# Kernel optimization log

Measured on AMD Instinct MI355X. Metric: run time of the kernel, lower is better.

## Reference

```python
import jax, jax.numpy as jnp
import numpy as np

B, T, TM = 4, 1024, 1500
D_MODEL, D_FFN, H, D_HEAD, D_MEM = 1024, 4096, 16, 64, 1024
EPS = 1e-5


def layernorm(x, g):
    m = jnp.mean(x, axis=-1, keepdims=True)
    xc = x - m
    v = jnp.mean(xc * xc, axis=-1, keepdims=True)
    return xc * jax.lax.rsqrt(v + EPS) * g


def setup_inputs() -> dict:
    key = jax.random.key(0)
    ks = jax.random.split(key, 12)
    s = lambda fan_in: 1.0 / np.sqrt(fan_in)
    return {
        "x": jax.random.normal(ks[0], (B, T, D_MODEL), jnp.float32),
        "encoder_output": jax.random.normal(ks[1], (B, TM, D_MEM), jnp.float32),
        "encoder_mask": jax.random.randint(ks[2], (B, TM), 0, 2).astype(bool),
        "w_qkv": jax.random.normal(ks[3], (D_MODEL, 3 * H * D_HEAD), jnp.float32) * s(D_MODEL),
        "w_o_sa": jax.random.normal(ks[4], (H * D_HEAD, D_MODEL), jnp.float32) * s(H * D_HEAD),
        "w_q": jax.random.normal(ks[5], (D_MODEL, H * D_HEAD), jnp.float32) * s(D_MODEL),
        "w_kv": jax.random.normal(ks[6], (D_MEM, 2 * H * D_HEAD), jnp.float32) * s(D_MEM),
        "w_o_xa": jax.random.normal(ks[7], (H * D_HEAD, D_MODEL), jnp.float32) * s(H * D_HEAD),
        "w_ff1": jax.random.normal(ks[8], (D_MODEL, D_FFN), jnp.float32) * s(D_MODEL),
        "w_ff2": jax.random.normal(ks[9], (D_FFN, D_MODEL), jnp.float32) * s(D_FFN),
        "g_sa": jnp.ones((D_MODEL,), jnp.float32),
        "g_xaq": jnp.ones((D_MODEL,), jnp.float32),
        "g_xam": jnp.ones((D_MEM,), jnp.float32),
        "g_ff": jnp.ones((D_MODEL,), jnp.float32),
    }


def reference(x, encoder_output, encoder_mask, w_qkv, w_o_sa, w_q, w_kv, w_o_xa,
              w_ff1, w_ff2, g_sa, g_xaq, g_xam, g_ff):
    b, t, _ = x.shape
    scale = D_HEAD ** -0.5

    # ---- causal self-attention ----
    residual = x
    xn = layernorm(x, g_sa)
    qkv = (xn @ w_qkv).reshape(b, t, 3, H, D_HEAD)
    q, k, v = qkv[:, :, 0], qkv[:, :, 1], qkv[:, :, 2]  # (B,T,H,D)
    scores = jnp.einsum('bqhd,bkhd->bhqk', q, k) * scale
    causal = jnp.tril(jnp.ones((t, t), x.dtype))
    scores = scores + (1.0 - causal) * -1e9
    attn = jax.nn.softmax(scores, axis=-1)
    sa = jnp.einsum('bhqk,bkhd->bqhd', attn, v).reshape(b, t, H * D_HEAD)
    x = residual + sa @ w_o_sa

    # ---- cross-attention ----
    residual = x
    qn = layernorm(x, g_xaq)
    mn = layernorm(encoder_output, g_xam)
    tq, tm = t, mn.shape[1]
    qx = (qn @ w_q).reshape(b, tq, H, D_HEAD)
    kvx = (mn @ w_kv).reshape(b, tm, 2, H, D_HEAD)
    kx, vx = kvx[:, :, 0], kvx[:, :, 1]
    xs = jnp.einsum('bqhd,bkhd->bhqk', qx, kx) * scale
    xs = jnp.where(encoder_mask[:, None, None, :], xs, -jnp.inf)
    xattn = jax.nn.softmax(xs, axis=-1)
    xa = jnp.einsum('bhqk,bkhd->bqhd', xattn, vx).reshape(b, tq, H * D_HEAD)
    x = residual + xa @ w_o_xa

    # ---- pointwise FFN (kernel_size=1 conv == linear) ----
    residual = x
    h = layernorm(x, g_ff)
    h = jax.nn.gelu(h @ w_ff1, approximate=True) @ w_ff2
    x = residual + h
    return (x, k, v)
```

## Files before the change

kernel.cpp:

```cpp
#include <hip/hip_runtime.h>
#include <hip/hip_bf16.h>
#include <cstdint>
#include <cstddef>


typedef __attribute__((ext_vector_type(4))) float f32x4;
typedef __attribute__((ext_vector_type(8))) short s8v;
typedef __attribute__((ext_vector_type(2))) unsigned uint2v;

#define DEVI __device__ __forceinline__

DEVI short f2bf(float f) {
  union { float f; unsigned u; } x; x.f = f;
  unsigned r = x.u + 0x7fffu + ((x.u >> 16) & 1u);
  return (short)(r >> 16);
}
DEVI unsigned cvtpk_bf2(float lo, float hi) {
  unsigned r;
  asm("v_cvt_pk_bf16_f32 %0, %1, %2" : "=v"(r) : "v"(lo), "v"(hi));
  return r;
}
DEVI float fexp2(float x) {
  float r;
  asm("v_exp_f32 %0, %1" : "=v"(r) : "v"(x));
  return r;
}
DEVI float bpermf(int srclane, float v) {
  union { float f; int i; } x; x.f = v;
  x.i = __builtin_amdgcn_ds_bpermute(srclane << 2, x.i);
  return x.f;
}
DEVI void gload_lds16(const void* g, void* l) {
  __builtin_amdgcn_global_load_lds((const __attribute__((address_space(1))) void*)g,
                                   (__attribute__((address_space(3))) void*)l,
                                   16, 0, 0);
}

DEVI void xcd_swizzle(int& bx, int& by) {
  int gx = gridDim.x, gy = gridDim.y;
  int nxy = gx * gy, chunk = nxy >> 3;
  int orig = blockIdx.y * gx + blockIdx.x;
  int gid = (orig & 7) * chunk + (orig >> 3);
  int full = gy << 3, nfull = gx >> 3, lim = nfull * full;
  if (gid < lim) {
    int band = gid / full, r = gid - band * full;
    bx = (band << 3) + (r & 7);
    by = r >> 3;
  } else {
    int r = gid - lim, w = gx - (nfull << 3);
    bx = (nfull << 3) + r % w;
    by = r / w;
  }
}

__global__ __launch_bounds__(256) void k_prep(
    const float* __restrict__ wqkv, const float* __restrict__ wosa,
    const float* __restrict__ wq,   const float* __restrict__ wkv,
    const float* __restrict__ woxa, const float* __restrict__ wff1,
    const float* __restrict__ wff2,
    short* __restrict__ wqkv_t, short* __restrict__ wosa_t,
    short* __restrict__ wq_t,   short* __restrict__ wkv_t,
    short* __restrict__ woxa_t, short* __restrict__ wff1_t,
    short* __restrict__ wff2_t,
    const int* __restrict__ mask, unsigned long long* __restrict__ mbits) {
  int id = blockIdx.x;
  const float* w; short* wt; int K, N, tx, r;
  if (id < 3072)       { w = wqkv; wt = wqkv_t; K = 1024; N = 3072; tx = 96;  r = id; }
  else if (id < 4096)  { w = wosa; wt = wosa_t; K = 1024; N = 1024; tx = 32;  r = id - 3072; }
  else if (id < 5120)  { w = wq;   wt = wq_t;   K = 1024; N = 1024; tx = 32;  r = id - 4096; }
  else if (id < 7168)  { w = wkv;  wt = wkv_t;  K = 1024; N = 2048; tx = 64;  r = id - 5120; }
  else if (id < 8192)  { w = woxa; wt = woxa_t; K = 1024; N = 1024; tx = 32;  r = id - 7168; }
  else if (id < 12288) { w = wff1; wt = wff1_t; K = 1024; N = 4096; tx = 128; r = id - 8192; }
  else if (id < 16384) { w = wff2; wt = wff2_t; K = 4096; N = 1024; tx = 32;  r = id - 12288; }
  else {
    int t = threadIdx.x;
    if (t < 96) {
      int b = t / 24, wd = t % 24;
      unsigned long long v = 0;
      const int* mb = mask + (size_t)b * 1500;
      for (int j = 0; j < 64; j++) {
        int k = wd * 64 + j;
        if (k < 1500 && mb[k]) v |= (1ull << j);
      }
      mbits[b * 24 + wd] = v;
    }
    return;
  }
  __shared__ float tile[32][33];
  int n0 = (r % tx) * 32, k0 = (r / tx) * 32;
  int t = threadIdx.x;
  int row = t >> 3, c4 = (t & 7) * 4;
  *(f32x4*)&tile[row][c4] = *(const f32x4*)(w + (size_t)(k0 + row) * N + n0 + c4);
  __syncthreads();
  float v0 = tile[c4 + 0][row], v1 = tile[c4 + 1][row];
  float v2 = tile[c4 + 2][row], v3 = tile[c4 + 3][row];
  uint2v o = {cvtpk_bf2(v0, v1), cvtpk_bf2(v2, v3)};
  *(uint2v*)(wt + (size_t)(n0 + row) * K + k0 + c4) = o;
}

__global__ __launch_bounds__(256) void k_vtrans(
    const short* __restrict__ src, int srs, int coff,
    short* __restrict__ dst, int T, int Tp) {
  __shared__ short tile[32][72];
  int bh = blockIdx.y, b = bh >> 4, h = bh & 15;
  int t0 = blockIdx.x * 32;
  const short* sB = src + (size_t)b * T * srs + coff + h * 64;
  short* dB = dst + (size_t)bh * 64 * Tp;
  int t = threadIdx.x;
  int r = t >> 3, c = (t & 7) * 8;
  int tr = t0 + r; if (tr > T - 1) tr = T - 1;
  *(s8v*)&tile[r][c] = *(const s8v*)(sB + (size_t)tr * srs + c);
  __syncthreads();
  int d = t & 63, ch = t >> 6;
  s8v o;
#pragma unroll
  for (int j = 0; j < 8; j++) o[j] = tile[ch * 8 + j][d];
  *(s8v*)(dB + (size_t)d * Tp + t0 + ch * 8) = o;
}

__global__ __launch_bounds__(256) void k_ln2(
    const float* __restrict__ x, const float* __restrict__ gx,
    short* __restrict__ ox,
    const float* __restrict__ e, const float* __restrict__ ge,
    short* __restrict__ oe) {
  int id = blockIdx.x;
  const float* src; const float* g; short* dst; int row;
  if (id < 4096) { src = x; g = gx; dst = ox; row = id; }
  else           { src = e; g = ge; dst = oe; row = id - 4096; }
  const float* xr = src + (size_t)row * 1024;
  int t = threadIdx.x, wid = t >> 6, lane = t & 63;
  f32x4 v = ((const f32x4*)xr)[t];
  float s = v[0] + v[1] + v[2] + v[3];
#pragma unroll
  for (int m = 32; m >= 1; m >>= 1) s += __shfl_xor(s, m);
  __shared__ float red[4];
  if (lane == 0) red[wid] = s;
  __syncthreads();
  float mean = (red[0] + red[1] + red[2] + red[3]) * (1.f / 1024.f);
  float q = 0.f;
#pragma unroll
  for (int i = 0; i < 4; i++) { v[i] -= mean; q += v[i] * v[i]; }
#pragma unroll
  for (int m = 32; m >= 1; m >>= 1) q += __shfl_xor(q, m);
  __syncthreads();
  if (lane == 0) red[wid] = q;
  __syncthreads();
  float var = (red[0] + red[1] + red[2] + red[3]) * (1.f / 1024.f);
  float rs = rsqrtf(var + 1e-5f);
  f32x4 gv = ((const f32x4*)g)[t];
  uint2v w = {cvtpk_bf2(v[0] * rs * gv[0], v[1] * rs * gv[1]),
              cvtpk_bf2(v[2] * rs * gv[2], v[3] * rs * gv[3])};
  *(uint2v*)(dst + (size_t)row * 1024 + t * 4) = w;
}

template <bool F32OUT, bool BF16OUT>
__global__ __launch_bounds__(256) void k_gemm3(
    const short* __restrict__ A, const short* __restrict__ Bt,
    float* __restrict__ Cf, short* __restrict__ Cb,
    int M, int N, int K, int lda, int ldb) {
  __shared__ short As[128 * 64];
  __shared__ short Bs[128 * 64];
  int z = blockIdx.z;
  A += (size_t)z * K;
  Bt += (size_t)z * K;
  if (F32OUT) Cf += (size_t)z * (size_t)M * N;

  int bx, by;
  xcd_swizzle(bx, by);
  int am = bx * 128, bn = by * 128;

  int t = threadIdx.x, wid = t >> 6, lane = t & 63;
  int la = lane & 15, lb = lane >> 4;
  int wr = wid >> 1, wc = wid & 1;

  const short* gp[8];
  int dof[8];
#pragma unroll
  for (int l = 0; l < 8; l++) {
    int cl = (l & 3) * 256 + t;
    int row = cl >> 3, g = cl & 7;
    int col = (g ^ (row & 7)) << 3;
    if (l < 4) {
      int ar = am + row; if (ar > M - 1) ar = M - 1;
      gp[l] = A + (size_t)ar * lda + col;
    } else {
      gp[l] = Bt + (size_t)(bn + row) * ldb + col;
    }
    dof[l] = ((l & 3) * 256 + wid * 64) * 8;
  }

  int aOff[4], bOff[4];
#pragma unroll
  for (int m = 0; m < 4; m++) {
    int r = wr * 64 + m * 16 + la;
    aOff[m] = r * 64 + ((lb ^ (r & 7)) << 3);
  }
#pragma unroll
  for (int n = 0; n < 4; n++) {
    int r = wc * 64 + n * 16 + la;
    bOff[n] = r * 64 + ((lb ^ (r & 7)) << 3);
  }

  f32x4 acc[4][4];
#pragma unroll
  for (int m = 0; m < 4; m++)
#pragma unroll
    for (int n = 0; n < 4; n++) acc[m][n] = (f32x4){0.f, 0.f, 0.f, 0.f};

  int nk = K >> 6;
  for (int ks = 0; ks < nk; ++ks) {
#pragma unroll
    for (int l = 0; l < 4; l++) { gload_lds16(gp[l], As + dof[l]); gp[l] += 64; }
#pragma unroll
    for (int l = 4; l < 8; l++) { gload_lds16(gp[l], Bs + dof[l]); gp[l] += 64; }
    __syncthreads();
#pragma unroll
    for (int kk = 0; kk < 2; kk++) {
      s8v af[4], bfg[4];
#pragma unroll
      for (int m = 0; m < 4; m++)
        af[m] = *(const s8v*)(As + (aOff[m] ^ (kk << 5)));
#pragma unroll
      for (int n = 0; n < 4; n++)
        bfg[n] = *(const s8v*)(Bs + (bOff[n] ^ (kk << 5)));
#pragma unroll
      for (int m = 0; m < 4; m++)
#pragma unroll
        for (int n = 0; n < 4; n++)
          acc[m][n] = __builtin_amdgcn_mfma_f32_16x16x32_bf16(af[m], bfg[n], acc[m][n], 0, 0, 0);
    }
    __syncthreads();
  }

#pragma unroll
  for (int m = 0; m < 4; m++) {
    int rb = am + wr * 64 + m * 16 + lb * 4;
#pragma unroll
    for (int n = 0; n < 4; n++) {
      int col = bn + wc * 64 + n * 16 + la;
#pragma unroll
      for (int j = 0; j < 4; j++) {
        int r = rb + j;
        if (r < M) {
          float v = acc[m][n][j];
          if (F32OUT) Cf[(size_t)r * N + col] = v;
          if (BF16OUT) Cb[(size_t)r * N + col] = f2bf(v);
        }
      }
    }
  }
}

template <bool GELU_, bool F32OUT, bool BF16OUT, bool KV>
__global__ __launch_bounds__(512) void k_gemm4(
    const short* __restrict__ A, const short* __restrict__ Bt,
    float* __restrict__ Cf, short* __restrict__ Cb,
    float* __restrict__ okv, int M, int N, int K, int lda, int ldb) {
  __shared__ short As[128 * 64];
  __shared__ short Bs[256 * 64];
  int z = blockIdx.z;
  A += (size_t)z * K;
  Bt += (size_t)z * K;
  if (F32OUT) Cf += (size_t)z * (size_t)M * N;

  int bx, by;
  xcd_swizzle(bx, by);
  int am = bx * 128, bn = by * 256;

  int t = threadIdx.x, wid = t >> 6, lane = t & 63;
  int la = lane & 15, lb = lane >> 4;
  int wr = wid >> 2, wc = wid & 3;

  const short* gpA[2]; const short* gpB[4];
  int dofA[2], dofB[4];
#pragma unroll
  for (int l = 0; l < 2; l++) {
    int c = l * 512 + t;
    int row = c >> 3, g = c & 7;
    int ar = am + row; if (ar > M - 1) ar = M - 1;
    gpA[l] = A + (size_t)ar * lda + ((g ^ (row & 7)) << 3);
    dofA[l] = (l * 512 + wid * 64) * 8;
  }
#pragma unroll
  for (int l = 0; l < 4; l++) {
    int c = l * 512 + t;
    int row = c >> 3, g = c & 7;
    gpB[l] = Bt + (size_t)(bn + row) * ldb + ((g ^ (row & 7)) << 3);
    dofB[l] = (l * 512 + wid * 64) * 8;
  }

  int aOff[4], bOff[4];
#pragma unroll
  for (int m = 0; m < 4; m++) {
    int r = wr * 64 + m * 16 + la;
    aOff[m] = r * 64 + ((lb ^ (r & 7)) << 3);
  }
#pragma unroll
  for (int n = 0; n < 4; n++) {
    int r = wc * 64 + n * 16 + la;
    bOff[n] = r * 64 + ((lb ^ (r & 7)) << 3);
  }

  f32x4 acc[4][4];
#pragma unroll
  for (int m = 0; m < 4; m++)
#pragma unroll
    for (int n = 0; n < 4; n++) acc[m][n] = (f32x4){0.f, 0.f, 0.f, 0.f};

  int nk = K >> 6;
  for (int ks = 0; ks < nk; ++ks) {
#pragma unroll
    for (int l = 0; l < 2; l++) { gload_lds16(gpA[l], As + dofA[l]); gpA[l] += 64; }
#pragma unroll
    for (int l = 0; l < 4; l++) { gload_lds16(gpB[l], Bs + dofB[l]); gpB[l] += 64; }
    __syncthreads();
#pragma unroll
    for (int kk = 0; kk < 2; kk++) {
      s8v af[4], bfg[4];
#pragma unroll
      for (int m = 0; m < 4; m++)
        af[m] = *(const s8v*)(As + (aOff[m] ^ (kk << 5)));
#pragma unroll
      for (int n = 0; n < 4; n++)
        bfg[n] = *(const s8v*)(Bs + (bOff[n] ^ (kk << 5)));
#pragma unroll
      for (int m = 0; m < 4; m++)
#pragma unroll
        for (int n = 0; n < 4; n++)
          acc[m][n] = __builtin_amdgcn_mfma_f32_16x16x32_bf16(af[m], bfg[n], acc[m][n], 0, 0, 0);
    }
    __syncthreads();
  }

#pragma unroll
  for (int m = 0; m < 4; m++) {
    int rb = am + wr * 64 + m * 16 + lb * 4;
#pragma unroll
    for (int n = 0; n < 4; n++) {
      int col = bn + wc * 64 + n * 16 + la;
#pragma unroll
      for (int j = 0; j < 4; j++) {
        int r = rb + j;
        if (r < M) {
          float v = acc[m][n][j];
          if (GELU_) {
            float u = v;
            float y = 0.7978845608f * u * (1.f + 0.044715f * u * u);
            float e = fexp2(fminf(y * 2.88539008f, 80.f));
            float th = (e - 1.f) * __builtin_amdgcn_rcpf(e + 1.f);
            v = 0.5f * u * (1.f + th);
          }
          if (F32OUT) Cf[(size_t)r * N + col] = v;
          if (BF16OUT) Cb[(size_t)r * N + col] = f2bf(v);
          if (KV) {
            if (col >= 2048)
              okv[(size_t)4096 * 1024 + (size_t)r * 1024 + (col - 2048)] = v;
            else if (col >= 1024)
              okv[(size_t)r * 1024 + (col - 1024)] = v;
          }
        }
      }
    }
  }
}

__global__ __launch_bounds__(256) void k_red2b(
    const f32x4* __restrict__ p, short* __restrict__ outb, int n) {
  int i = blockIdx.x * 256 + threadIdx.x;
  f32x4 v = p[i] + p[i + (size_t)n];
  uint2v w = {cvtpk_bf2(v[0], v[1]), cvtpk_bf2(v[2], v[3])};
  *(uint2v*)(outb + (size_t)i * 4) = w;
}

__global__ __launch_bounds__(256) void k_red4(
    const f32x4* __restrict__ p, const f32x4* __restrict__ res,
    float* __restrict__ outf, int n) {
  int i = blockIdx.x * 256 + threadIdx.x;
  f32x4 v = res[i] + ((p[i] + p[i + (size_t)n]) +
                      (p[i + 2 * (size_t)n] + p[i + 3 * (size_t)n]));
  ((f32x4*)outf)[i] = v;
}

__global__ __launch_bounds__(256) void k_red2ln(
    const f32x4* __restrict__ p, const f32x4* __restrict__ res,
    float* __restrict__ xout, short* __restrict__ nout,
    const float* __restrict__ g, int n) {
  int row = blockIdx.x;
  int t = threadIdx.x, wid = t >> 6, lane = t & 63;
  size_t i = (size_t)row * 256 + t;
  f32x4 v = res[i] + (p[i] + p[i + (size_t)n]);
  ((f32x4*)xout)[i] = v;
  float s = v[0] + v[1] + v[2] + v[3];
#pragma unroll
  for (int m = 32; m >= 1; m >>= 1) s += __shfl_xor(s, m);
  __shared__ float red[4];
  if (lane == 0) red[wid] = s;
  __syncthreads();
  float mean = (red[0] + red[1] + red[2] + red[3]) * (1.f / 1024.f);
  float q = 0.f;
#pragma unroll
  for (int k = 0; k < 4; k++) { v[k] -= mean; q += v[k] * v[k]; }
#pragma unroll
  for (int m = 32; m >= 1; m >>= 1) q += __shfl_xor(q, m);
  __syncthreads();
  if (lane == 0) red[wid] = q;
  __syncthreads();
  float var = (red[0] + red[1] + red[2] + red[3]) * (1.f / 1024.f);
  float rs = rsqrtf(var + 1e-5f);
  f32x4 gv = ((const f32x4*)g)[t];
  uint2v w = {cvtpk_bf2(v[0] * rs * gv[0], v[1] * rs * gv[1]),
              cvtpk_bf2(v[2] * rs * gv[2], v[3] * rs * gv[3])};
  *(uint2v*)(nout + (size_t)row * 1024 + t * 4) = w;
}

template <bool CAUSAL>
__global__ __launch_bounds__(512) void k_attn4(
    const short* __restrict__ qbuf, int qrs,
    const short* __restrict__ kbuf, int krs,
    const short* __restrict__ vT, int vts,
    short* __restrict__ obuf, int ors,
    const unsigned long long* __restrict__ mbits, int mwords,
    int Tq, int Tk, float scale) {
  __shared__ short Ks[64 * 64];
  __shared__ short Vs[64 * 64];
  __shared__ short Ps[8 * 1024];
  int lid = blockIdx.y * gridDim.x + blockIdx.x;
  int rest = lid >> 3;
  int bh = (lid & 7) * 8 + (rest & 7);
  int qsel = rest >> 3;
  int b = bh >> 4, h = bh & 15;
  int t = threadIdx.x, wid = t >> 6, lane = t & 63;
  int la = lane & 15, lb = lane >> 4;
  float lscale = scale * 1.44269504f;

  const short* qB = qbuf + (size_t)b * Tq * qrs + h * 64;
  const short* kB = kbuf + (size_t)b * Tk * krs + h * 64;
  const short* vB = vT + (size_t)bh * 64 * vts;
  char* Pw = (char*)(Ps + wid * 1024);

  int sr = t >> 3, scol = (t & 7) * 8;
  int swz = sr * 64 + (scol ^ ((sr & 7) << 3));

  int nsup = CAUSAL ? 2 : 1;
  for (int s = 0; s < nsup; s++) {
    int st = CAUSAL ? (s ? 7 - qsel : qsel) : qsel;
    int q0 = st * 128 + wid * 16;
    int nkt = CAUSAL ? 2 * st + 2 : (Tk + 63) >> 6;
    int lastkt = CAUSAL ? (q0 >> 6) : nkt - 1;

    s8v qf[2];
#pragma unroll
    for (int kk = 0; kk < 2; kk++)
      qf[kk] = *(const s8v*)(qB + (size_t)(q0 + la) * qrs + kk * 32 + lb * 8);

    f32x4 accO[4];
#pragma unroll
    for (int n = 0; n < 4; n++) accO[n] = (f32x4){0.f, 0.f, 0.f, 0.f};
    float m = -1e30f, l = 0.f;

    s8v krg, vrg;
    {
      int tk = sr; if (tk > Tk - 1) tk = Tk - 1;
      krg = *(const s8v*)(kB + (size_t)tk * krs + scol);
      vrg = *(const s8v*)(vB + (size_t)sr * vts + scol);
    }

    for (int kt = 0; kt < nkt; kt++) {
      int kb0 = kt << 6;
      __syncthreads();
      *(s8v*)&Ks[swz] = krg;
      *(s8v*)&Vs[swz] = vrg;
      __syncthreads();
      if (kt + 1 < nkt) {
        int kb = kb0 + 64;
        int tk = kb + sr; if (tk > Tk - 1) tk = Tk - 1;
        krg = *(const s8v*)(kB + (size_t)tk * krs + scol);
        vrg = *(const s8v*)(vB + (size_t)sr * vts + kb + scol);
      }
      if (kt > lastkt) continue;

      bool needMask;
      unsigned long long wm = ~0ull;
      if (CAUSAL) {
        needMask = (kt == lastkt);
      } else {
        wm = mbits[(size_t)b * mwords + kt];
        needMask = (wm != ~0ull);
      }

      float sc[4][4];
      __builtin_amdgcn_s_setprio(1);
#pragma unroll
      for (int n = 0; n < 4; n++) {
        f32x4 a = (f32x4){0.f, 0.f, 0.f, 0.f};
#pragma unroll
        for (int kk = 0; kk < 2; kk++) {
          s8v kf = *(const s8v*)&Ks[(n * 16 + la) * 64 +
                                    ((kk * 32 + lb * 8) ^ ((la & 7) << 3))];
          a = __builtin_amdgcn_mfma_f32_16x16x32_bf16(kf, qf[kk], a, 0, 0, 0);
        }
#pragma unroll
        for (int j = 0; j < 4; j++) {
          float sv = a[j] * lscale;
          if (needMask) {
            int ki = n * 16 + lb * 4 + j;
            bool ok = CAUSAL ? (kb0 + ki <= q0 + la) : (((wm >> ki) & 1ull) != 0);
            sv = ok ? sv : -1e30f;
          }
          sc[n][j] = sv;
        }
      }
      __builtin_amdgcn_s_setprio(0);

      float tm = sc[0][0];
#pragma unroll
      for (int n = 0; n < 4; n++)
#pragma unroll
        for (int j = 0; j < 4; j++) tm = fmaxf(tm, sc[n][j]);
      tm = fmaxf(tm, __shfl_xor(tm, 16));
      tm = fmaxf(tm, __shfl_xor(tm, 32));
      tm = fmaxf(tm, -1e4f);

      bool skip = __all(tm - m <= 10.f);
      float alpha = 1.f;
      if (!skip) {
        float mn_ = fmaxf(m, tm);
        alpha = fexp2(m - mn_);
        m = mn_;
      }

      unsigned W[4][2];
      float ps = 0.f;
#pragma unroll
      for (int n = 0; n < 4; n++) {
        float p0 = fexp2(sc[n][0] - m), p1 = fexp2(sc[n][1] - m);
        float p2 = fexp2(sc[n][2] - m), p3 = fexp2(sc[n][3] - m);
        ps += (p0 + p1) + (p2 + p3);
        W[n][0] = cvtpk_bf2(p0, p1);
        W[n][1] = cvtpk_bf2(p2, p3);
      }
      ps += __shfl_xor(ps, 16);
      ps += __shfl_xor(ps, 32);
      l = l * alpha + ps;

      if (!skip) {
#pragma unroll
        for (int j = 0; j < 4; j++) {
          float aj = bpermf(lb * 20 + j, alpha);
#pragma unroll
          for (int n = 0; n < 4; n++) accO[n][j] *= aj;
        }
      }

#pragma unroll
      for (int n = 0; n < 4; n++) {
        uint2v w2 = {W[n][0], W[n][1]};
        *(uint2v*)(Pw + ((la * 128 + n * 32 + lb * 8) ^ ((la & 7) << 4))) = w2;
      }
      __builtin_amdgcn_s_setprio(1);
#pragma unroll
      for (int kk = 0; kk < 2; kk++) {
        s8v pa = *(const s8v*)(Pw + ((la * 128 + kk * 64 + lb * 16) ^ ((la & 7) << 4)));
#pragma unroll
        for (int n = 0; n < 4; n++) {
          s8v vf = *(const s8v*)&Vs[(n * 16 + la) * 64 +
                                    ((kk * 32 + lb * 8) ^ ((la & 7) << 3))];
          accO[n] = __builtin_amdgcn_mfma_f32_16x16x32_bf16(pa, vf, accO[n], 0, 0, 0);
        }
      }
      __builtin_amdgcn_s_setprio(0);
    }

#pragma unroll
    for (int j = 0; j < 4; j++) {
      float lj = bpermf(lb * 20 + j, l);
      float inv = 1.f / lj;
      int r = q0 + lb * 4 + j;
#pragma unroll
      for (int n = 0; n < 4; n++)
        obuf[(size_t)(b * Tq + r) * ors + h * 64 + n * 16 + la] = f2bf(accO[n][j] * inv);
    }
  }
}

extern "C" void kernel_launch(void* const* d_in, const int* in_sizes, int n_in,
                              void* d_out, int out_size, void* d_ws, size_t ws_size,
                              hipStream_t stream) {
  (void)in_sizes; (void)n_in; (void)out_size; (void)ws_size;
  const float* x      = (const float*)d_in[0];
  const float* enc    = (const float*)d_in[1];
  const int*   mask   = (const int*)d_in[2];
  const float* w_qkv  = (const float*)d_in[3];
  const float* w_o_sa = (const float*)d_in[4];
  const float* w_q    = (const float*)d_in[5];
  const float* w_kv   = (const float*)d_in[6];
  const float* w_o_xa = (const float*)d_in[7];
  const float* w_ff1  = (const float*)d_in[8];
  const float* w_ff2  = (const float*)d_in[9];
  const float* g_sa   = (const float*)d_in[10];
  const float* g_xaq  = (const float*)d_in[11];
  const float* g_xam  = (const float*)d_in[12];
  const float* g_ff   = (const float*)d_in[13];

  float* out_x = (float*)d_out;
  float* out_k = out_x + (size_t)4096 * 1024;

  char* ws = (char*)d_ws;
  size_t off = 0;
  auto alloc = [&](size_t bytes) -> void* {
    void* p = ws + off;
    off += (bytes + 255) & ~(size_t)255;
    return p;
  };
  short* wqkv_t = (short*)alloc((size_t)3072 * 1024 * 2);
  short* wosa_t = (short*)alloc((size_t)1024 * 1024 * 2);
  short* wq_t   = (short*)alloc((size_t)1024 * 1024 * 2);
  short* wkv_t  = (short*)alloc((size_t)2048 * 1024 * 2);
  short* woxa_t = (short*)alloc((size_t)1024 * 1024 * 2);
  short* wff1_t = (short*)alloc((size_t)4096 * 1024 * 2);
  short* wff2_t = (short*)alloc((size_t)1024 * 4096 * 2);
  short* xn     = (short*)alloc((size_t)4096 * 1024 * 2);
  short* qkv_b  = (short*)alloc((size_t)4096 * 3072 * 2);
  short* sa_b   = (short*)alloc((size_t)4096 * 1024 * 2);
  float* x1     = (float*)alloc((size_t)4096 * 1024 * 4);
  short* qn     = (short*)alloc((size_t)4096 * 1024 * 2);
  short* mn     = (short*)alloc((size_t)6000 * 1024 * 2);
  short* qx_b   = (short*)alloc((size_t)4096 * 1024 * 2);
  short* kvx_b  = (short*)alloc((size_t)6000 * 2048 * 2);
  short* xa_b   = (short*)alloc((size_t)4096 * 1024 * 2);
  float* x2     = (float*)alloc((size_t)4096 * 1024 * 4);
  short* hn     = (short*)alloc((size_t)4096 * 1024 * 2);
  short* h1     = (short*)alloc((size_t)4096 * 4096 * 2);
  unsigned long long* mbits = (unsigned long long*)alloc(4 * 24 * 8);

  short* vTsa = xn;
  short* vTxa = h1;
  float* partH = (float*)h1;
  float* partQ = (float*)qkv_b;
  const int NRED = 1048576;

  k_prep<<<16385, 256, 0, stream>>>(
      w_qkv, w_o_sa, w_q, w_kv, w_o_xa, w_ff1, w_ff2,
      wqkv_t, wosa_t, wq_t, wkv_t, woxa_t, wff1_t, wff2_t, mask, mbits);
  k_ln2<<<10096, 256, 0, stream>>>(x, g_sa, xn, enc, g_xam, mn);

  k_gemm4<false, false, true, true><<<dim3(32, 12), 512, 0, stream>>>(
      xn, wqkv_t, nullptr, qkv_b, out_k, 4096, 3072, 1024, 1024, 1024);
  k_vtrans<<<dim3(32, 64), 256, 0, stream>>>(qkv_b, 3072, 2048, vTsa, 1024, 1024);
  k_attn4<true><<<dim3(4, 64), 512, 0, stream>>>(
      qkv_b, 3072, qkv_b + 1024, 3072, vTsa, 1024,
      sa_b, 1024, nullptr, 0, 1024, 1024, 0.125f);
  k_gemm3<true, false><<<dim3(32, 8, 2), 256, 0, stream>>>(
      sa_b, wosa_t, partH, nullptr, 4096, 1024, 512, 1024, 1024);
  k_red2ln<<<4096, 256, 0, stream>>>(
      (const f32x4*)partH, (const f32x4*)x, x1, qn, g_xaq, NRED);

  k_gemm3<true, false><<<dim3(32, 8, 2), 256, 0, stream>>>(
      qn, wq_t, partH, nullptr, 4096, 1024, 512, 1024, 1024);
  k_red2b<<<4096, 256, 0, stream>>>((const f32x4*)partH, qx_b, NRED);
  k_gemm4<false, false, true, false><<<dim3(47, 8), 512, 0, stream>>>(
      mn, wkv_t, nullptr, kvx_b, nullptr, 6000, 2048, 1024, 1024, 1024);
  k_vtrans<<<dim3(48, 64), 256, 0, stream>>>(kvx_b, 2048, 1024, vTxa, 1500, 1536);
  k_attn4<false><<<dim3(8, 64), 512, 0, stream>>>(
      qx_b, 1024, kvx_b, 2048, vTxa, 1536,
      xa_b, 1024, mbits, 24, 1024, 1500, 0.125f);
  k_gemm3<true, false><<<dim3(32, 8, 2), 256, 0, stream>>>(
      xa_b, woxa_t, partH, nullptr, 4096, 1024, 512, 1024, 1024);
  k_red2ln<<<4096, 256, 0, stream>>>(
      (const f32x4*)partH, (const f32x4*)x1, x2, hn, g_ff, NRED);

  k_gemm4<true, false, true, false><<<dim3(32, 16), 512, 0, stream>>>(
      hn, wff1_t, nullptr, h1, nullptr, 4096, 4096, 1024, 1024, 1024);
  k_gemm4<false, true, false, false><<<dim3(32, 4, 4), 512, 0, stream>>>(
      h1, wff2_t, partQ, nullptr, nullptr, 4096, 1024, 1024, 4096, 4096);
  k_red4<<<4096, 256, 0, stream>>>(
      (const f32x4*)partQ, (const f32x4*)x2, out_x, NRED);
}
```

Measured before the change: 391.4 us.

## Widen attention key tile to 128 and defer softmax scaling into exp FMA

The attention kernel now processes 128 keys per iteration instead of 64, which halves the number of barrier/LDS-staging rounds and online-softmax rescale steps per query block. K and V shared buffers double in size, and V uses a new XOR swizzle for its 128-wide rows. The score scaling moves out of the per-element path: the row max uses v_max3 on raw scores, and scaling is folded into an FMA before exp2. The causal path drops per-warp tile skipping, so some warps may compute fully masked halves. The change also raises register pressure from the larger score array.

```diff
diff --git a/kernel.cpp b/kernel.cpp
--- a/kernel.cpp
+++ b/kernel.cpp
@@ -23,6 +23,11 @@
 DEVI float fexp2(float x) {
   float r;
   asm("v_exp_f32 %0, %1" : "=v"(r) : "v"(x));
+  return r;
+}
+DEVI float fmax3(float a, float b, float c) {
+  float r;
+  asm("v_max3_f32 %0, %1, %2, %3" : "=v"(r) : "v"(a), "v"(b), "v"(c));
   return r;
 }
 DEVI float bpermf(int srclane, float v) {
@@ -421,8 +426,8 @@
     short* __restrict__ obuf, int ors,
     const unsigned long long* __restrict__ mbits, int mwords,
     int Tq, int Tk, float scale) {
-  __shared__ short Ks[64 * 64];
-  __shared__ short Vs[64 * 64];
+  __shared__ short Ks[128 * 64];
+  __shared__ short Vs[64 * 128];
   __shared__ short Ps[8 * 1024];
   int lid = blockIdx.y * gridDim.x + blockIdx.x;
   int rest = lid >> 3;
@@ -438,15 +443,15 @@
   const short* vB = vT + (size_t)bh * 64 * vts;
   char* Pw = (char*)(Ps + wid * 1024);
 
-  int sr = t >> 3, scol = (t & 7) * 8;
-  int swz = sr * 64 + (scol ^ ((sr & 7) << 3));
+  int sr = t >> 3, g0 = t & 7, scol = g0 * 8;
+  int kswz = sr * 64 + ((g0 ^ (sr & 7)) << 3);
+  int vswz = sr * 128 + ((g0 ^ (sr & 7)) << 3);
 
   int nsup = CAUSAL ? 2 : 1;
   for (int s = 0; s < nsup; s++) {
     int st = CAUSAL ? (s ? 7 - qsel : qsel) : qsel;
     int q0 = st * 128 + wid * 16;
-    int nkt = CAUSAL ? 2 * st + 2 : (Tk + 63) >> 6;
-    int lastkt = CAUSAL ? (q0 >> 6) : nkt - 1;
+    int nkt = CAUSAL ? st + 1 : (Tk + 127) >> 7;
 
     s8v qf[2];
 #pragma unroll
@@ -458,40 +463,48 @@
     for (int n = 0; n < 4; n++) accO[n] = (f32x4){0.f, 0.f, 0.f, 0.f};
     float m = -1e30f, l = 0.f;
 
-    s8v krg, vrg;
+    s8v krg0, krg1, vrg0, vrg1;
     {
-      int tk = sr; if (tk > Tk - 1) tk = Tk - 1;
-      krg = *(const s8v*)(kB + (size_t)tk * krs + scol);
-      vrg = *(const s8v*)(vB + (size_t)sr * vts + scol);
+      int tk0 = sr; if (tk0 > Tk - 1) tk0 = Tk - 1;
+      int tk1 = 64 + sr; if (tk1 > Tk - 1) tk1 = Tk - 1;
+      krg0 = *(const s8v*)(kB + (size_t)tk0 * krs + scol);
+      krg1 = *(const s8v*)(kB + (size_t)tk1 * krs + scol);
+      vrg0 = *(const s8v*)(vB + (size_t)sr * vts + scol);
+      vrg1 = *(const s8v*)(vB + (size_t)sr * vts + 64 + scol);
     }
 
     for (int kt = 0; kt < nkt; kt++) {
-      int kb0 = kt << 6;
+      int kb0 = kt << 7;
       __syncthreads();
-      *(s8v*)&Ks[swz] = krg;
-      *(s8v*)&Vs[swz] = vrg;
+      *(s8v*)&Ks[kswz] = krg0;
+      *(s8v*)&Ks[kswz + 64 * 64] = krg1;
+      *(s8v*)&Vs[vswz] = vrg0;
+      *(s8v*)&Vs[vswz + 64] = vrg1;
       __syncthreads();
       if (kt + 1 < nkt) {
-        int kb = kb0 + 64;
-        int tk = kb + sr; if (tk > Tk - 1) tk = Tk - 1;
-        krg = *(const s8v*)(kB + (size_t)tk * krs + scol);
-        vrg = *(const s8v*)(vB + (size_t)sr * vts + kb + scol);
-      }
-      if (kt > lastkt) continue;
+        int kb = kb0 + 128;
+        int tk0 = kb + sr; if (tk0 > Tk - 1) tk0 = Tk - 1;
+        int tk1 = kb + 64 + sr; if (tk1 > Tk - 1) tk1 = Tk - 1;
+        krg0 = *(const s8v*)(kB + (size_t)tk0 * krs + scol);
+        krg1 = *(const s8v*)(kB + (size_t)tk1 * krs + scol);
+        vrg0 = *(const s8v*)(vB + (size_t)sr * vts + kb + scol);
+        vrg1 = *(const s8v*)(vB + (size_t)sr * vts + kb + 64 + scol);
+      }
 
       bool needMask;
-      unsigned long long wm = ~0ull;
+      unsigned long long wm0 = ~0ull, wm1 = ~0ull;
       if (CAUSAL) {
-        needMask = (kt == lastkt);
+        needMask = (kt == nkt - 1);
       } else {
-        wm = mbits[(size_t)b * mwords + kt];
-        needMask = (wm != ~0ull);
-      }
-
-      float sc[4][4];
+        wm0 = mbits[(size_t)b * mwords + 2 * kt];
+        wm1 = mbits[(size_t)b * mwords + 2 * kt + 1];
+        needMask = ((wm0 & wm1) != ~0ull);
+      }
+
+      float sc[8][4];
       __builtin_amdgcn_s_setprio(1);
 #pragma unroll
-      for (int n = 0; n < 4; n++) {
+      for (int n = 0; n < 8; n++) {
         f32x4 a = (f32x4){0.f, 0.f, 0.f, 0.f};
 #pragma unroll
         for (int kk = 0; kk < 2; kk++) {
@@ -499,27 +512,31 @@
                                     ((kk * 32 + lb * 8) ^ ((la & 7) << 3))];
           a = __builtin_amdgcn_mfma_f32_16x16x32_bf16(kf, qf[kk], a, 0, 0, 0);
         }
-#pragma unroll
-        for (int j = 0; j < 4; j++) {
-          float sv = a[j] * lscale;
-          if (needMask) {
+        if (needMask) {
+          unsigned long long wmn = (n < 4) ? wm0 : wm1;
+#pragma unroll
+          for (int j = 0; j < 4; j++) {
             int ki = n * 16 + lb * 4 + j;
-            bool ok = CAUSAL ? (kb0 + ki <= q0 + la) : (((wm >> ki) & 1ull) != 0);
-            sv = ok ? sv : -1e30f;
+            bool ok = CAUSAL ? (kb0 + ki <= q0 + la)
+                             : (((wmn >> ((n & 3) * 16 + lb * 4 + j)) & 1ull) != 0);
+            sc[n][j] = ok ? a[j] : -1e30f;
           }
-          sc[n][j] = sv;
+        } else {
+#pragma unroll
+          for (int j = 0; j < 4; j++) sc[n][j] = a[j];
         }
       }
       __builtin_amdgcn_s_setprio(0);
 
-      float tm = sc[0][0];
-#pragma unroll
-      for (int n = 0; n < 4; n++)
-#pragma unroll
-        for (int j = 0; j < 4; j++) tm = fmaxf(tm, sc[n][j]);
+      float rn[8];
+#pragma unroll
+      for (int n = 0; n < 8; n++)
+        rn[n] = fmaxf(fmax3(sc[n][0], sc[n][1], sc[n][2]), sc[n][3]);
+      float tm = fmax3(fmax3(rn[0], rn[1], rn[2]), fmax3(rn[3], rn[4], rn[5]),
+                       fmaxf(rn[6], rn[7]));
       tm = fmaxf(tm, __shfl_xor(tm, 16));
       tm = fmaxf(tm, __shfl_xor(tm, 32));
-      tm = fmaxf(tm, -1e4f);
+      tm = fmaxf(tm * lscale, -1e4f);
 
       bool skip = __all(tm - m <= 10.f);
       float alpha = 1.f;
@@ -528,13 +545,16 @@
         alpha = fexp2(m - mn_);
         m = mn_;
       }
-
-      unsigned W[4][2];
+      float nm = -m;
+
+      unsigned W[8][2];
       float ps = 0.f;
 #pragma unroll
-      for (int n = 0; n < 4; n++) {
-        float p0 = fexp2(sc[n][0] - m), p1 = fexp2(sc[n][1] - m);
-        float p2 = fexp2(sc[n][2] - m), p3 = fexp2(sc[n][3] - m);
+      for (int n = 0; n < 8; n++) {
+        float p0 = fexp2(__builtin_fmaf(sc[n][0], lscale, nm));
+        float p1 = fexp2(__builtin_fmaf(sc[n][1], lscale, nm));
+        float p2 = fexp2(__builtin_fmaf(sc[n][2], lscale, nm));
+        float p3 = fexp2(__builtin_fmaf(sc[n][3], lscale, nm));
         ps += (p0 + p1) + (p2 + p3);
         W[n][0] = cvtpk_bf2(p0, p1);
         W[n][1] = cvtpk_bf2(p2, p3);
@@ -553,22 +573,26 @@
       }
 
 #pragma unroll
-      for (int n = 0; n < 4; n++) {
-        uint2v w2 = {W[n][0], W[n][1]};
-        *(uint2v*)(Pw + ((la * 128 + n * 32 + lb * 8) ^ ((la & 7) << 4))) = w2;
-      }
-      __builtin_amdgcn_s_setprio(1);
-#pragma unroll
-      for (int kk = 0; kk < 2; kk++) {
-        s8v pa = *(const s8v*)(Pw + ((la * 128 + kk * 64 + lb * 16) ^ ((la & 7) << 4)));
-#pragma unroll
-        for (int n = 0; n < 4; n++) {
-          s8v vf = *(const s8v*)&Vs[(n * 16 + la) * 64 +
-                                    ((kk * 32 + lb * 8) ^ ((la & 7) << 3))];
-          accO[n] = __builtin_amdgcn_mfma_f32_16x16x32_bf16(pa, vf, accO[n], 0, 0, 0);
+      for (int hf = 0; hf < 2; hf++) {
+#pragma unroll
+        for (int n2 = 0; n2 < 4; n2++) {
+          uint2v w2 = {W[hf * 4 + n2][0], W[hf * 4 + n2][1]};
+          *(uint2v*)(Pw + ((la * 128 + n2 * 32 + lb * 8) ^ ((la & 7) << 4))) = w2;
         }
-      }
-      __builtin_amdgcn_s_setprio(0);
+        __builtin_amdgcn_s_setprio(1);
+#pragma unroll
+        for (int kk2 = 0; kk2 < 2; kk2++) {
+          s8v pa = *(const s8v*)(Pw + ((la * 128 + kk2 * 64 + lb * 16) ^ ((la & 7) << 4)));
+          int kkg = hf * 2 + kk2;
+#pragma unroll
+          for (int n = 0; n < 4; n++) {
+            s8v vf = *(const s8v*)&Vs[(n * 16 + la) * 128 +
+                                      (((kkg * 4 + lb) ^ (la & 7)) << 3)];
+            accO[n] = __builtin_amdgcn_mfma_f32_16x16x32_bf16(pa, vf, accO[n], 0, 0, 0);
+          }
+        }
+        __builtin_amdgcn_s_setprio(0);
+      }
     }
 
 #pragma unroll
```

Measured after the change: 396.6 us. Within noise of the previous version (+1.3%).
